# Kernel tuning notes

Measured on AMD Instinct MI355X. Metric: run time of the kernel, lower is better.

## Reference

```python
import jax, jax.numpy as jnp
import numpy as np

D = 1024

def setup_inputs() -> dict:
    key = jax.random.key(0)
    ks = jax.random.split(key, 9)
    B, S = 4, 2048
    s = 1.0 / np.sqrt(D)
    return {
        "query": jax.random.normal(ks[0], (B, S, D), jnp.float32),
        "key": jax.random.normal(ks[1], (B, S, D), jnp.float32),
        "value": jax.random.normal(ks[2], (B, S, D), jnp.float32),
        "Wq": jax.random.normal(ks[3], (D, D), jnp.float32) * s,
        "bq": jax.random.normal(ks[4], (D,), jnp.float32) * 0.01,
        "Wk": jax.random.normal(ks[5], (D, D), jnp.float32) * s,
        "bk": jax.random.normal(ks[6], (D,), jnp.float32) * 0.01,
        "Wv": jax.random.normal(ks[7], (D, D), jnp.float32) * s,
        "bv": jax.random.normal(ks[8], (D,), jnp.float32) * 0.01,
    }

def reference(query, key, value, Wq, bq, Wk, bk, Wv, bv):
    scale = 1.0 / (query.shape[-1] ** 0.5)
    q = jnp.einsum('bsd,ed->bse', query, Wq) + bq  # nn.Linear: x @ W.T + b
    k = jnp.einsum('bsd,ed->bse', key, Wk) + bk
    v = jnp.einsum('bsd,ed->bse', value, Wv) + bv
    scores = jnp.einsum('bqd,bkd->bqk', q, k) * scale  # [B, Sq, Skv]
    w = jax.nn.softmax(scores, axis=-1)
    return jnp.einsum('bqk,bkd->bqd', w, v)
```

## Files before the change

kernel.cpp:

```cpp
#include <hip/hip_runtime.h>

typedef __bf16 bf16x8 __attribute__((ext_vector_type(8)));
typedef float f32x4 __attribute__((ext_vector_type(4)));
typedef unsigned short u16x8 __attribute__((ext_vector_type(8)));

__device__ inline unsigned short f2bf(float f) {
  union { float f; unsigned u; } a; a.f = f;
  return (unsigned short)((a.u + 0x7fffu + ((a.u >> 16) & 1u)) >> 16);
}
__device__ inline float bf2f(unsigned short h) {
  union { unsigned u; float f; } a; a.u = ((unsigned)h) << 16;
  return a.f;
}

__global__ __launch_bounds__(256) void cvtW(const float* __restrict__ Wq,
                                            const float* __restrict__ Wk,
                                            const float* __restrict__ Wv,
                                            unsigned short* __restrict__ Wb) {
  int i = blockIdx.x * 256 + threadIdx.x;
  int idx = i >> 18;
  int off = i & 262143;
  const float* s = (idx == 0) ? Wq : ((idx == 1) ? Wk : Wv);
  float4 v = ((const float4*)s)[off];
  ushort4 o;
  o.x = f2bf(v.x); o.y = f2bf(v.y); o.z = f2bf(v.z); o.w = f2bf(v.w);
  ((ushort4*)(Wb + idx * 1048576))[off] = o;
}

#define G2L(gp, lp) __builtin_amdgcn_global_load_lds( \
    (const __attribute__((address_space(1))) void*)(gp), \
    (__attribute__((address_space(3))) void*)(lp), 16, 0, 0)

#define MFMA_(d, a, b) d = __builtin_amdgcn_mfma_f32_16x16x32_bf16(a, b, d, 0, 0, 0)
#define SB0() __builtin_amdgcn_sched_barrier(0)
#define LGKM(n) do { asm volatile("s_waitcnt lgkmcnt(" #n ")" ::: "memory"); SB0(); } while (0)
#define VMC(n) do { asm volatile("s_waitcnt vmcnt(" #n ")" ::: "memory"); SB0(); } while (0)

struct PJ {
  const float* A0; const float* A1; const float* A2;
  const unsigned short* B;
  unsigned short* outQ; unsigned short* outK; unsigned short* outV;
  const float* biasQ; const float* biasK; const float* biasV;
};

__global__ __launch_bounds__(256, 2) void gemmP(PJ p) {
  extern __shared__ char smem[];
  char* smA = smem;
  char* smB = smem + 65536;
  const int tid = threadIdx.x, lane = tid & 63, wid = tid >> 6;
  const int wm = wid;

  int orig = blockIdx.x + 8 * (blockIdx.y + 32 * blockIdx.z);
  int wg = (orig & 7) * 96 + (orig >> 3);
  int bx = wg & 7; int t2 = wg >> 3; int by = t2 & 31; int z = t2 >> 5;
  const int m0 = by << 8, n0 = bx << 7;

  const float* Az = (z == 0) ? p.A0 : ((z == 1) ? p.A1 : p.A2);

  const int sgA = (tid & 7) ^ ((tid >> 3) & 7);
  const char* srcA = (const char*)Az
      + ((long long)m0 + 2 * (tid >> 3) + (sgA >> 2)) * 4096 + ((sgA & 3) << 4);
  const char* srcB = (const char*)(p.B + (long long)z * 1048576)
      + ((long long)n0 + 2 * (tid >> 3) + (sgA >> 2)) * 2048 + ((sgA & 3) << 4);

  const int kh = lane >> 4;
  const int Ra0 = (wm << 6) + (lane & 15);
  const int aJ = (kh >> 1) << 14;
  const int kq0 = (kh & 1) << 1;
  const int Rb0 = lane & 15;

  f32x4 acc[4][8];
#pragma unroll
  for (int i = 0; i < 4; ++i)
#pragma unroll
    for (int j = 0; j < 8; ++j) acc[i][j] = (f32x4){0.f, 0.f, 0.f, 0.f};

  f32x4 aLoF[2][2], aHiF[2][2];
  bf16x8 aLoB[2], aHiB[2], bLo[4], bHi[4];

  auto stage = [&](int t) {
    char* dA = smA + ((t & 1) << 15) + (tid << 4);
    char* dB = smB + ((t & 1) << 13) + (tid << 4);
    const char* sA = srcA + (long long)t * 128;
    const char* sB = srcB + (long long)t * 64;
#pragma unroll
    for (int c = 0; c < 8; ++c)
      G2L(sA + (long long)(c & 3) * 64 * 4096 + ((c >> 2) << 6), dA + (c << 12));
#pragma unroll
    for (int c = 0; c < 2; ++c)
      G2L(sB + (long long)c * 64 * 2048, dB + (c << 12));
  };
  auto readA = [&](int b, int half, f32x4 (&dst)[2][2]) {
    const char* ra = smA + (b << 15) + aJ;
#pragma unroll
    for (int f = 0; f < 2; ++f) {
      const int R = Ra0 + ((half * 2 + f) << 4);
      const int lineB = (R >> 1) << 7;
      const int x = ((R & 1) << 2) ^ ((R >> 1) & 7);
      dst[f][0] = *(const f32x4*)(ra + lineB + ((x ^ (kq0 | 0)) << 4));
      dst[f][1] = *(const f32x4*)(ra + lineB + ((x ^ (kq0 | 1)) << 4));
    }
  };
  auto readB = [&](int b, int half, bf16x8 (&dst)[4]) {
    const char* rb = smB + (b << 13);
#pragma unroll
    for (int f = 0; f < 4; ++f) {
      const int R = Rb0 + ((half * 4 + f) << 4);
      const int byte = ((R >> 1) << 7)
                     + (((((R & 1) << 2) | kh) ^ ((R >> 1) & 7)) << 4);
      dst[f] = *(const bf16x8*)(rb + byte);
    }
  };
  auto cvtA = [&](f32x4 (&s)[2][2], bf16x8 (&d)[2]) {
#pragma unroll
    for (int f = 0; f < 2; ++f)
      d[f] = (bf16x8){(__bf16)s[f][0][0], (__bf16)s[f][0][1],
                      (__bf16)s[f][0][2], (__bf16)s[f][0][3],
                      (__bf16)s[f][1][0], (__bf16)s[f][1][1],
                      (__bf16)s[f][1][2], (__bf16)s[f][1][3]};
  };
  auto quadP = [&](int qa, int qb, bf16x8 (&A)[2], bf16x8 (&B)[4]) {
    __builtin_amdgcn_s_setprio(1);
#pragma unroll
    for (int mi = 0; mi < 2; ++mi)
#pragma unroll
      for (int ni = 0; ni < 4; ++ni)
        MFMA_(acc[qa * 2 + mi][qb * 4 + ni], A[mi], B[ni]);
    __builtin_amdgcn_s_setprio(0);
  };

  stage(0);
  VMC(0);
  __builtin_amdgcn_s_barrier();
  readA(0, 0, aLoF); readB(0, 0, bLo);
  SB0();

  const int NT = 32;
  for (int t = 0; t < NT; ++t) {
    if (t + 1 < NT) stage(t + 1);
    readA(t & 1, 1, aHiF);
    SB0();
    LGKM(4);
    cvtA(aLoF, aLoB);
    quadP(0, 0, aLoB, bLo);
    readB(t & 1, 1, bHi);
    SB0();
    LGKM(4);
    cvtA(aHiF, aHiB);
    quadP(1, 0, aHiB, bLo);
    LGKM(0);
    quadP(0, 1, aLoB, bHi);
    quadP(1, 1, aHiB, bHi);
    VMC(0);
    __builtin_amdgcn_s_barrier();
    if (t + 1 < NT) { readA((t + 1) & 1, 0, aLoF); readB((t + 1) & 1, 0, bLo); }
    SB0();
  }

  const int c0 = lane & 15, r0 = (lane >> 4) << 2;
  if (z < 2) {
    unsigned short* O = (z == 0) ? p.outQ : p.outK;
    const float* bias = (z == 0) ? p.biasQ : p.biasK;
#pragma unroll
    for (int mi = 0; mi < 4; ++mi) {
      const int grow = m0 + (wm << 6) + (mi << 4) + r0;
#pragma unroll
      for (int ni = 0; ni < 8; ++ni) {
        const int gcol = n0 + (ni << 4) + c0;
        const float bb = bias[gcol];
#pragma unroll
        for (int rr = 0; rr < 4; ++rr)
          O[(long long)(grow + rr) * 1024 + gcol] = f2bf(acc[mi][ni][rr] + bb);
      }
    }
  } else {
#pragma unroll
    for (int mi = 0; mi < 4; ++mi) {
      const int grow = m0 + (wm << 6) + (mi << 4) + r0;
      const int bb = grow >> 11, s = grow & 2047;
#pragma unroll
      for (int ni = 0; ni < 8; ++ni) {
        const int d = n0 + (ni << 4) + c0;
        const float ba = p.biasV[d];
        ushort4 pk;
        pk.x = f2bf(acc[mi][ni][0] + ba);
        pk.y = f2bf(acc[mi][ni][1] + ba);
        pk.z = f2bf(acc[mi][ni][2] + ba);
        pk.w = f2bf(acc[mi][ni][3] + ba);
        *(ushort4*)(p.outV + ((long long)bb << 21) + (long long)d * 2048 + s) = pk;
      }
    }
  }
}

#define EPI_SCALE 1
#define EPI_OUT 2

struct GP {
  const unsigned short* A;
  const unsigned short* B;
  unsigned short* C;
  long long batchA, batchB, batchC;
  int lda, ldb, ldc, K;
  float scale;
};

template<int BM, int BN, int WMW, int WNW, int EPI>
__global__ __launch_bounds__(512, 2) void gemm2(GP p) {
  constexpr int NWN = BN / WNW;
  constexpr int AMF = WMW / 16, BNF = WNW / 16;
  constexpr int AH = AMF / 2, BH = BNF / 2;
  constexpr int AF_N = AH * 2;
  constexpr int NBA = BM / 64, NBB = BN / 64;
  static_assert((BM / WMW) * NWN == 8, "8 waves");
  static_assert(BNF == 4, "lgkm immediates assume BNF==4");

  extern __shared__ char smem[];
  char* smA = smem;
  char* smB = smem + 2 * BM * 128;

  const int tid = threadIdx.x;
  const int lane = tid & 63;
  const int wid = tid >> 6;
  const int wm = wid / NWN, wn = wid % NWN;

  const int gx = gridDim.x, gy = gridDim.y;
  const int nwg = gx * gy * (int)gridDim.z;
  int orig = blockIdx.x + gx * (blockIdx.y + gy * blockIdx.z);
  int qq = nwg >> 3, rr_ = nwg & 7;
  int xcd = orig & 7, sl = orig >> 3;
  int wg = (xcd < rr_ ? xcd * (qq + 1) : rr_ * (qq + 1) + (xcd - rr_) * qq) + sl;
  int bx = wg % gx;
  int t2 = wg / gx;
  int by = t2 % gy;
  int z  = t2 / gy;

  const int m0 = by * BM, n0 = bx * BN;

  const long long lda2 = (long long)p.lda * 2;
  const long long ldb2 = (long long)p.ldb * 2;
  const char* Abase = (const char*)(p.A + (long long)z * p.batchA) + (long long)m0 * lda2;
  const char* Bbase = (const char*)(p.B + (long long)z * p.batchB) + (long long)n0 * ldb2;

  const int trow = tid >> 3;
  const int cs = (((tid & 7) ^ (trow & 7)) << 4);
  const char* srcA = Abase + (long long)trow * lda2 + cs;
  const char* srcB = Bbase + (long long)trow * ldb2 + cs;

  const int NT = p.K >> 6;

  const int aRowB = ((wm * WMW + (lane & 15)) << 7);
  const int bRowB = ((wn * WNW + (lane & 15)) << 7);
  const int csw = (lane & 7) << 4;
  const int ck0 = (((lane >> 4) << 4)) ^ csw;
  const int ck1 = ((((lane >> 4) << 4)) | 64) ^ csw;

  f32x4 acc[AMF][BNF];
#pragma unroll
  for (int i = 0; i < AMF; ++i)
#pragma unroll
    for (int j = 0; j < BNF; ++j) acc[i][j] = (f32x4){0.f, 0.f, 0.f, 0.f};

  bf16x8 aLo[AH][2], aHi[AH][2], bLo[BH][2], bHi[BH][2];

  auto stage = [&](int t) {
    char* dA = smA + (t & 1) * (BM * 128) + (tid << 4);
    char* dB = smB + (t & 1) * (BN * 128) + (tid << 4);
    const char* sA = srcA + (long long)t * 128;
    const char* sB = srcB + (long long)t * 128;
#pragma unroll
    for (int c = 0; c < NBA; ++c) G2L(sA + (long long)c * (lda2 << 6), dA + c * 8192);
#pragma unroll
    for (int c = 0; c < NBB; ++c) G2L(sB + (long long)c * (ldb2 << 6), dB + c * 8192);
  };
  auto readAh = [&](int t, int half, bf16x8 (&dst)[AH][2]) {
    const char* ra = smA + (t & 1) * (BM * 128) + aRowB + half * (AH * 2048);
#pragma unroll
    for (int mi = 0; mi < AH; ++mi) {
      dst[mi][0] = *(const bf16x8*)(ra + mi * 2048 + ck0);
      dst[mi][1] = *(const bf16x8*)(ra + mi * 2048 + ck1);
    }
  };
  auto readBh = [&](int t, int half, bf16x8 (&dst)[BH][2]) {
    const char* rb = smB + (t & 1) * (BN * 128) + bRowB + half * (BH * 2048);
#pragma unroll
    for (int ni = 0; ni < BH; ++ni) {
      dst[ni][0] = *(const bf16x8*)(rb + ni * 2048 + ck0);
      dst[ni][1] = *(const bf16x8*)(rb + ni * 2048 + ck1);
    }
  };
  auto quad = [&](int qa, int qb, bf16x8 (&A)[AH][2], bf16x8 (&B)[BH][2]) {
    __builtin_amdgcn_s_setprio(1);
#pragma unroll
    for (int mi = 0; mi < AH; ++mi)
#pragma unroll
      for (int ni = 0; ni < BH; ++ni) {
        MFMA_(acc[qa * AH + mi][qb * BH + ni], A[mi][0], B[ni][0]);
        MFMA_(acc[qa * AH + mi][qb * BH + ni], A[mi][1], B[ni][1]);
      }
    __builtin_amdgcn_s_setprio(0);
  };

  stage(0); stage(1);
  if constexpr (NBA + NBB == 8) VMC(8); else VMC(6);
  __builtin_amdgcn_s_barrier();
  readAh(0, 0, aLo); readBh(0, 0, bLo);
  SB0();

  for (int t = 0; t < NT; ++t) {
    readAh(t, 1, aHi);
    SB0();
    if constexpr (AF_N == 8) LGKM(8); else LGKM(4);
    quad(0, 0, aLo, bLo);
    readBh(t, 1, bHi);
    SB0();
    LGKM(4);
    quad(1, 0, aHi, bLo);
    LGKM(0);
    quad(0, 1, aLo, bHi);
    quad(1, 1, aHi, bHi);
    VMC(0);
    __builtin_amdgcn_s_barrier();
    if (t + 2 < NT) stage(t + 2);
    if (t + 1 < NT) { readAh(t + 1, 0, aLo); readBh(t + 1, 0, bLo); }
    SB0();
  }

  const int c0 = lane & 15;
  const int r0 = (lane >> 4) << 2;
  if constexpr (EPI == EPI_SCALE) {
    unsigned short* Cz = p.C + (long long)z * p.batchC;
#pragma unroll
    for (int mi = 0; mi < AMF; ++mi) {
      const int grow = m0 + wm * WMW + (mi << 4) + r0;
#pragma unroll
      for (int ni = 0; ni < BNF; ++ni) {
        const int gcol = n0 + wn * WNW + (ni << 4) + c0;
#pragma unroll
        for (int rr = 0; rr < 4; ++rr)
          Cz[(long long)(grow + rr) * p.ldc + gcol] = f2bf(acc[mi][ni][rr] * p.scale);
      }
    }
  } else {
    float* Cz = (float*)p.C + (long long)z * p.batchC;
#pragma unroll
    for (int mi = 0; mi < AMF; ++mi) {
      const int grow = m0 + wm * WMW + (mi << 4) + r0;
#pragma unroll
      for (int ni = 0; ni < BNF; ++ni) {
        const int gcol = n0 + wn * WNW + (ni << 4) + c0;
#pragma unroll
        for (int rr = 0; rr < 4; ++rr)
          Cz[(long long)(grow + rr) * p.ldc + gcol] = acc[mi][ni][rr] * p.scale;
      }
    }
  }
}

__global__ __launch_bounds__(256) void softmax_rows(unsigned short* __restrict__ S) {
  const size_t row = blockIdx.x;
  unsigned short* pp = S + row * 2048;
  const int t = threadIdx.x, lane = t & 63, wave = t >> 6;
  u16x8 h = ((const u16x8*)pp)[t];
  float x[8];
#pragma unroll
  for (int j = 0; j < 8; ++j) x[j] = bf2f(h[j]);
  float m = x[0];
#pragma unroll
  for (int j = 1; j < 8; ++j) m = fmaxf(m, x[j]);
#pragma unroll
  for (int off = 32; off >= 1; off >>= 1) m = fmaxf(m, __shfl_xor(m, off, 64));
  __shared__ float rmax[4], rsum[4];
  if (lane == 0) rmax[wave] = m;
  __syncthreads();
  m = fmaxf(fmaxf(rmax[0], rmax[1]), fmaxf(rmax[2], rmax[3]));
  float e[8], sum = 0.f;
#pragma unroll
  for (int j = 0; j < 8; ++j) { e[j] = __expf(x[j] - m); sum += e[j]; }
#pragma unroll
  for (int off = 32; off >= 1; off >>= 1) sum += __shfl_xor(sum, off, 64);
  if (lane == 0) rsum[wave] = sum;
  __syncthreads();
  sum = rsum[0] + rsum[1] + rsum[2] + rsum[3];
  const float inv = 1.f / sum;
  u16x8 o;
#pragma unroll
  for (int j = 0; j < 8; ++j) o[j] = f2bf(e[j] * inv);
  ((u16x8*)pp)[t] = o;
}

extern "C" void kernel_launch(void* const* d_in, const int* in_sizes, int n_in,
                              void* d_out, int out_size, void* d_ws, size_t ws_size,
                              hipStream_t stream) {
  const float* q  = (const float*)d_in[0];
  const float* k  = (const float*)d_in[1];
  const float* v  = (const float*)d_in[2];
  const float* Wq = (const float*)d_in[3];
  const float* bq = (const float*)d_in[4];
  const float* Wk = (const float*)d_in[5];
  const float* bk = (const float*)d_in[6];
  const float* Wv = (const float*)d_in[7];
  const float* bv = (const float*)d_in[8];

  unsigned short* S  = (unsigned short*)d_ws;
  unsigned short* Wb = S + 16777216;
  unsigned short* qb = Wb + 3145728;
  unsigned short* kb = qb + 8388608;
  unsigned short* vT = kb + 8388608;

  (void)hipFuncSetAttribute((const void*)gemmP,
      hipFuncAttributeMaxDynamicSharedMemorySize, 81920);
  (void)hipFuncSetAttribute((const void*)gemm2<256,256,128,64,EPI_SCALE>,
      hipFuncAttributeMaxDynamicSharedMemorySize, 131072);
  (void)hipFuncSetAttribute((const void*)gemm2<256,128,64,64,EPI_OUT>,
      hipFuncAttributeMaxDynamicSharedMemorySize, 98304);

  cvtW<<<3072, 256, 0, stream>>>(Wq, Wk, Wv, Wb);

  PJ pj{};
  pj.A0 = q; pj.A1 = k; pj.A2 = v;
  pj.B = Wb;
  pj.outQ = qb; pj.outK = kb; pj.outV = vT;
  pj.biasQ = bq; pj.biasK = bk; pj.biasV = bv;
  gemmP<<<dim3(8, 32, 3), 256, 81920, stream>>>(pj);

  GP gs{};
  gs.A = qb; gs.batchA = 2097152; gs.lda = 1024;
  gs.B = kb; gs.batchB = 2097152; gs.ldb = 1024;
  gs.C = S;  gs.batchC = 4194304; gs.ldc = 2048;
  gs.K = 1024; gs.scale = 0.03125f;
  gemm2<256,256,128,64,EPI_SCALE><<<dim3(8, 8, 4), 512, 131072, stream>>>(gs);

  softmax_rows<<<8192, 256, 0, stream>>>(S);

  GP gv{};
  gv.A = S;  gv.batchA = 4194304; gv.lda = 2048;
  gv.B = vT; gv.batchB = 2097152; gv.ldb = 2048;
  gv.C = (unsigned short*)d_out; gv.batchC = 2097152; gv.ldc = 1024;
  gv.K = 2048; gv.scale = 1.f;
  gemm2<256,128,64,64,EPI_OUT><<<dim3(8, 8, 4), 512, 98304, stream>>>(gv);
}
```

Measured before the change: 176.7 us.

## Convert fp32 A tiles to bf16 before LDS and deepen projection pipeline

The projection GEMM no longer copies fp32 activations straight into LDS. It now loads them into registers, converts them to bf16 and writes bf16 to LDS, which halves LDS footprint and LDS read traffic for the A operand and removes the per-MFMA conversion. Loads now run two K-steps ahead, with a three-buffer ring for B and register double-buffering for A. LDS per block drops from 80KB to 56KB. In exchange, the launch-bounds occupancy hint is dropped and more VGPRs are spent on register staging, which may lower occupancy.

```diff
diff --git a/kernel.cpp b/kernel.cpp
--- a/kernel.cpp
+++ b/kernel.cpp
@@ -43,10 +43,10 @@
   const float* biasQ; const float* biasK; const float* biasV;
 };
 
-__global__ __launch_bounds__(256, 2) void gemmP(PJ p) {
+__global__ __launch_bounds__(256) void gemmP(PJ p) {
   extern __shared__ char smem[];
   char* smA = smem;
-  char* smB = smem + 65536;
+  char* smB = smem + 32768;
   const int tid = threadIdx.x, lane = tid & 63, wid = tid >> 6;
   const int wm = wid;
 
@@ -57,16 +57,19 @@
 
   const float* Az = (z == 0) ? p.A0 : ((z == 1) ? p.A1 : p.A2);
 
-  const int sgA = (tid & 7) ^ ((tid >> 3) & 7);
-  const char* srcA = (const char*)Az
-      + ((long long)m0 + 2 * (tid >> 3) + (sgA >> 2)) * 4096 + ((sgA & 3) << 4);
-  const char* srcB = (const char*)(p.B + (long long)z * 1048576)
-      + ((long long)n0 + 2 * (tid >> 3) + (sgA >> 2)) * 2048 + ((sgA & 3) << 4);
+  const char* srcA0 = (const char*)Az + ((long long)m0 + (tid >> 3)) * 4096
+                    + ((tid & 7) << 4);
+  const int L0 = tid >> 3;
+  const int sgB = (tid & 7) ^ (L0 & 7);
+  const char* srcB = (const char*)(p.B + (long long)z * 1048576
+                     + (long long)(n0 + 2 * L0 + (sgB >> 2)) * 1024)
+                   + ((sgB & 3) << 4);
+
+  const int kqW = (tid & 7) >> 1;
+  const int hW = (tid & 1) << 3;
 
   const int kh = lane >> 4;
   const int Ra0 = (wm << 6) + (lane & 15);
-  const int aJ = (kh >> 1) << 14;
-  const int kq0 = (kh & 1) << 1;
   const int Rb0 = lane & 15;
 
   f32x4 acc[4][8];
@@ -75,30 +78,43 @@
 #pragma unroll
     for (int j = 0; j < 8; ++j) acc[i][j] = (f32x4){0.f, 0.f, 0.f, 0.f};
 
-  f32x4 aLoF[2][2], aHiF[2][2];
-  bf16x8 aLoB[2], aHiB[2], bLo[4], bHi[4];
-
-  auto stage = [&](int t) {
-    char* dA = smA + ((t & 1) << 15) + (tid << 4);
-    char* dB = smB + ((t & 1) << 13) + (tid << 4);
-    const char* sA = srcA + (long long)t * 128;
+  float4 aregA[8], aregB[8];
+  bf16x8 aLo[2], aHi[2], bLo[4], bHi[4];
+
+  auto ldA = [&](int t, float4 (&ar)[8]) {
+    const char* s = srcA0 + (long long)t * 128;
+#pragma unroll
+    for (int c = 0; c < 8; ++c)
+      ar[c] = *(const float4*)(s + (long long)c * 32 * 4096);
+  };
+  auto wrA = [&](int t, float4 (&ar)[8]) {
+    char* dA = smA + ((t & 1) << 14);
+#pragma unroll
+    for (int c = 0; c < 8; ++c) {
+      const int rc = (c << 5) + (tid >> 3);
+      const int line = rc >> 1, par = rc & 1;
+      float4 v = ar[c];
+      union { __bf16 b[4]; unsigned long long u; } o;
+      o.b[0] = (__bf16)v.x; o.b[1] = (__bf16)v.y;
+      o.b[2] = (__bf16)v.z; o.b[3] = (__bf16)v.w;
+      *(unsigned long long*)(dA + (line << 7)
+          + ((((par << 2) | kqW) ^ (line & 7)) << 4) + hW) = o.u;
+    }
+  };
+  auto stageB = [&](int t, int b) {
+    char* dB = smB + (b << 13) + (tid << 4);
     const char* sB = srcB + (long long)t * 64;
-#pragma unroll
-    for (int c = 0; c < 8; ++c)
-      G2L(sA + (long long)(c & 3) * 64 * 4096 + ((c >> 2) << 6), dA + (c << 12));
 #pragma unroll
     for (int c = 0; c < 2; ++c)
       G2L(sB + (long long)c * 64 * 2048, dB + (c << 12));
   };
-  auto readA = [&](int b, int half, f32x4 (&dst)[2][2]) {
-    const char* ra = smA + (b << 15) + aJ;
+  auto readA = [&](int b, int half, bf16x8 (&dst)[2]) {
+    const char* ra = smA + (b << 14);
 #pragma unroll
     for (int f = 0; f < 2; ++f) {
       const int R = Ra0 + ((half * 2 + f) << 4);
-      const int lineB = (R >> 1) << 7;
-      const int x = ((R & 1) << 2) ^ ((R >> 1) & 7);
-      dst[f][0] = *(const f32x4*)(ra + lineB + ((x ^ (kq0 | 0)) << 4));
-      dst[f][1] = *(const f32x4*)(ra + lineB + ((x ^ (kq0 | 1)) << 4));
+      dst[f] = *(const bf16x8*)(ra + ((R >> 1) << 7)
+               + (((((R & 1) << 2) | kh) ^ ((R >> 1) & 7)) << 4));
     }
   };
   auto readB = [&](int b, int half, bf16x8 (&dst)[4]) {
@@ -106,18 +122,9 @@
 #pragma unroll
     for (int f = 0; f < 4; ++f) {
       const int R = Rb0 + ((half * 4 + f) << 4);
-      const int byte = ((R >> 1) << 7)
-                     + (((((R & 1) << 2) | kh) ^ ((R >> 1) & 7)) << 4);
-      dst[f] = *(const bf16x8*)(rb + byte);
-    }
-  };
-  auto cvtA = [&](f32x4 (&s)[2][2], bf16x8 (&d)[2]) {
-#pragma unroll
-    for (int f = 0; f < 2; ++f)
-      d[f] = (bf16x8){(__bf16)s[f][0][0], (__bf16)s[f][0][1],
-                      (__bf16)s[f][0][2], (__bf16)s[f][0][3],
-                      (__bf16)s[f][1][0], (__bf16)s[f][1][1],
-                      (__bf16)s[f][1][2], (__bf16)s[f][1][3]};
+      dst[f] = *(const bf16x8*)(rb + ((R >> 1) << 7)
+               + (((((R & 1) << 2) | kh) ^ ((R >> 1) & 7)) << 4));
+    }
   };
   auto quadP = [&](int qa, int qb, bf16x8 (&A)[2], bf16x8 (&B)[4]) {
     __builtin_amdgcn_s_setprio(1);
@@ -129,33 +136,42 @@
     __builtin_amdgcn_s_setprio(0);
   };
 
-  stage(0);
-  VMC(0);
+  const int NT = 32;
+  int b0 = 0, b1 = 1, b2 = 2;
+
+  ldA(0, aregA); stageB(0, 0);
+  ldA(1, aregB); stageB(1, 1);
+  VMC(10);
+  wrA(0, aregA);
+  LGKM(0);
   __builtin_amdgcn_s_barrier();
-  readA(0, 0, aLoF); readB(0, 0, bLo);
+  readA(0, 0, aLo); readB(0, 0, bLo);
   SB0();
 
-  const int NT = 32;
-  for (int t = 0; t < NT; ++t) {
-    if (t + 1 < NT) stage(t + 1);
-    readA(t & 1, 1, aHiF);
+  auto body = [&](int t, float4 (&arW)[8], float4 (&arL)[8]) {
+    const bool pf1 = (t + 1) < NT, pf2 = (t + 2) < NT;
+    if (pf2) { ldA(t + 2, arL); stageB(t + 2, b2); }
+    readA(t & 1, 1, aHi);
+    SB0();
+    LGKM(2);
+    quadP(0, 0, aLo, bLo);
+    readB(b0, 1, bHi);
     SB0();
     LGKM(4);
-    cvtA(aLoF, aLoB);
-    quadP(0, 0, aLoB, bLo);
-    readB(t & 1, 1, bHi);
-    SB0();
-    LGKM(4);
-    cvtA(aHiF, aHiB);
-    quadP(1, 0, aHiB, bLo);
+    quadP(1, 0, aHi, bLo);
     LGKM(0);
-    quadP(0, 1, aLoB, bHi);
-    quadP(1, 1, aHiB, bHi);
-    VMC(0);
+    quadP(0, 1, aLo, bHi);
+    quadP(1, 1, aHi, bHi);
+    if (pf2)      { VMC(10); }
+    else          { VMC(0);  }
+    if (pf1) wrA(t + 1, arW);
+    LGKM(0);
     __builtin_amdgcn_s_barrier();
-    if (t + 1 < NT) { readA((t + 1) & 1, 0, aLoF); readB((t + 1) & 1, 0, bLo); }
-    SB0();
-  }
+    if (pf1) { readA((t + 1) & 1, 0, aLo); readB(b1, 0, bLo); }
+    SB0();
+    int tmp = b0; b0 = b1; b1 = b2; b2 = tmp;
+  };
+  for (int t = 0; t < NT; t += 2) { body(t, aregB, aregA); body(t + 1, aregA, aregB); }
 
   const int c0 = lane & 15, r0 = (lane >> 4) << 2;
   if (z < 2) {
@@ -409,7 +425,7 @@
   unsigned short* vT = kb + 8388608;
 
   (void)hipFuncSetAttribute((const void*)gemmP,
-      hipFuncAttributeMaxDynamicSharedMemorySize, 81920);
+      hipFuncAttributeMaxDynamicSharedMemorySize, 57344);
   (void)hipFuncSetAttribute((const void*)gemm2<256,256,128,64,EPI_SCALE>,
       hipFuncAttributeMaxDynamicSharedMemorySize, 131072);
   (void)hipFuncSetAttribute((const void*)gemm2<256,128,64,64,EPI_OUT>,
@@ -422,7 +438,7 @@
   pj.B = Wb;
   pj.outQ = qb; pj.outK = kb; pj.outV = vT;
   pj.biasQ = bq; pj.biasK = bk; pj.biasV = bv;
-  gemmP<<<dim3(8, 32, 3), 256, 81920, stream>>>(pj);
+  gemmP<<<dim3(8, 32, 3), 256, 57344, stream>>>(pj);
 
   GP gs{};
   gs.A = qb; gs.batchA = 2097152; gs.lda = 1024;
```

After: 205.4 us. 16.3% more time.
